# Performance work log

Hardware: AMD Instinct MI355X
Metric: run time of the kernel (lower is better)

## Reference

```python
import jax, jax.numpy as jnp
import numpy as np

B, C, H, W = 32, 4, 512, 512
T = 64  # Angular_representive_Threshold
GROUPS = 2


def setup_inputs() -> dict:
    key = jax.random.key(0)
    k1, k2 = jax.random.split(key)
    x_real = jax.random.normal(k1, (B, C, H, W), dtype=jnp.float32)
    x_imag = jax.random.normal(k2, (B, C, H, W), dtype=jnp.float32)
    return {"x_real": x_real, "x_imag": x_imag}


def reference(x_real, x_imag):
    # Complex angular-delay input, split into 2 groups of 2 channels (torch.chunk dim=1)
    x = (x_real + 1j * x_imag).astype(jnp.complex64)            # [B,4,H,W]
    xg = x.reshape(B, GROUPS, 2, H, W)                          # [B,g,ch,H,W]
    ch0, ch1 = xg[:, :, 0], xg[:, :, 1]                         # [B,g,H,W]
    # sqrt(|real|^2) == |real|; energy difference summed over delay axis H (dim=2)
    diff = (jnp.abs(jnp.abs(ch0.real) - jnp.abs(ch1.imag)) +
            jnp.abs(jnp.abs(ch1.real) - jnp.abs(ch0.imag))).sum(axis=2)  # [B,g,W]
    # torch.sort ascending, keep first T indices (smallest energy difference)
    idx = jnp.argsort(diff, axis=-1)[..., :T]                   # [B,g,T]
    # vectorized column scatter replacing the per-batch/per-threshold python loops
    mask = jnp.zeros((B, GROUPS, W), jnp.float32).at[
        jnp.arange(B)[:, None, None],
        jnp.arange(GROUPS)[None, :, None],
        idx].set(1.0)                                           # [B,g,W]
    xm = xg * mask[:, :, None, None, :]                         # zero non-selected angular bins
    # ifft over delay (dim=-2) then fft over angle (dim=-1), +0.5 on real part
    out = jnp.fft.fft(jnp.fft.ifft(xm, axis=-2), axis=-1) + 0.5
    out = out.reshape(B, C, H, W).astype(jnp.complex64)         # concat of both groups on dim=1
    # return as stacked real/imag float32 (complex64 payload)
    return jnp.stack([out.real, out.imag], axis=-1)             # [B,4,H,W,2]
```

## Files before the change

### kernel.cpp

```cpp
#include <hip/hip_runtime.h>
#include <math.h>

#define NB 32
#define NC 4
#define NH 512
#define NW 512
#define NT 64
#define NG 2
#define BK 32

typedef __attribute__((ext_vector_type(8))) short short8;
typedef __attribute__((ext_vector_type(4))) short short4v;
typedef __attribute__((ext_vector_type(4))) float float4v;

__device__ inline unsigned short f2bf(float f) {
  union { float f; unsigned u; } v; v.f = f;
  unsigned r = v.u + 0x7FFF + ((v.u >> 16) & 1);
  return (unsigned short)(r >> 16);
}

__device__ __forceinline__ void gld16(const unsigned short* g, unsigned short* l) {
  __builtin_amdgcn_global_load_lds(
      (__attribute__((address_space(1))) const unsigned int*)g,
      (__attribute__((address_space(3))) unsigned int*)l, 16, 0, 0);
}

__global__ __launch_bounds__(256) void k_diff(const float* __restrict__ xr,
                                              const float* __restrict__ xi,
                                              float* __restrict__ diffp) {
  int bg = blockIdx.x, hc = blockIdx.y;
  int b = bg >> 1, g = bg & 1;
  size_t c0 = ((size_t)(b * NC + 2 * g)) * NH * NW;
  size_t c1 = c0 + (size_t)NH * NW;
  int t = threadIdx.x;
  int q = t & 127, rg = t >> 7;
  int h0 = hc * 64;
  float4v acc = {0.f, 0.f, 0.f, 0.f};
  for (int r = rg; r < 64; r += 2) {
    size_t o = (size_t)(h0 + r) * NW + q * 4;
    float4v r0 = *(const float4v*)(xr + c0 + o);
    float4v i0 = *(const float4v*)(xi + c0 + o);
    float4v r1 = *(const float4v*)(xr + c1 + o);
    float4v i1 = *(const float4v*)(xi + c1 + o);
#pragma unroll
    for (int k = 0; k < 4; ++k)
      acc[k] += fabsf(fabsf(r0[k]) - fabsf(i1[k])) + fabsf(fabsf(r1[k]) - fabsf(i0[k]));
  }
  __shared__ float4v red[256];
  red[t] = acc;
  __syncthreads();
  if (t < 128) {
    float4v v = red[t];
    float4v u = red[t + 128];
#pragma unroll
    for (int k = 0; k < 4; ++k) v[k] += u[k];
    *(float4v*)(diffp + ((size_t)hc * 64 + bg) * NW + q * 4) = v;
  }
}

__global__ void k_select(const float* __restrict__ diffp, int* __restrict__ sel) {
  __shared__ float v[NW];
  int w = threadIdx.x;
  int bg = blockIdx.x;
  float mine = 0.f;
#pragma unroll
  for (int hc = 0; hc < 8; ++hc) mine += diffp[((size_t)hc * 64 + bg) * NW + w];
  v[w] = mine;
  __syncthreads();
  int rank = 0;
  for (int u = 0; u < NW; ++u) {
    float o = v[u];
    rank += (o < mine) || (o == mine && u < w);
  }
  if (rank < NT) sel[bg * NT + rank] = w;
}

__global__ __launch_bounds__(256) void k_build_T(unsigned short* __restrict__ Tb) {
  __shared__ float2 lt[512];
  int t = threadIdx.x;
  {
    float s, c;
    sincosf(6.2831853071795864769f * (float)t * (1.0f / 512.0f), &s, &c);
    lt[t] = make_float2(c, s);
    sincosf(6.2831853071795864769f * (float)(t + 256) * (1.0f / 512.0f), &s, &c);
    lt[t + 256] = make_float2(c, s);
  }
  __syncthreads();
#pragma unroll
  for (int i = 0; i < 4; ++i) {
    int idx = blockIdx.x * 1024 + i * 256 + t;
    int m = idx >> 10, k = idx & 1023;
    int hm = m & 511, rm = m >> 9;
    int hk = k & 511, rk = k >> 9;
    float2 cs = lt[(hm * hk) & 511];
    float val = (rm == rk) ? cs.x : (rk ? -cs.y : cs.y);
    Tb[idx] = f2bf(val * (1.0f / 512.0f));
  }
}

__global__ __launch_bounds__(256) void k_gather(const float* __restrict__ xr,
                                                const float* __restrict__ xi,
                                                const int* __restrict__ sel,
                                                unsigned short* __restrict__ Xg) {
  __shared__ short jmap[512];
  __shared__ __align__(16) unsigned short tile[2][64][136];
  int img = blockIdx.x, hc = blockIdx.y;
  int t = threadIdx.x;
  int b = img >> 2, g = (img >> 1) & 1;
  jmap[t] = -1;
  jmap[t + 256] = -1;
  __syncthreads();
  if (t < NT) {
    int w = sel[(b * NG + g) * NT + t];
    jmap[w] = (short)t;
  }
  __syncthreads();
  size_t base = (size_t)img * NH * NW + (size_t)hc * 128 * NW;
  for (int i = 0; i < 64; ++i) {
    int lin = i * 256 + t;
    int r = lin >> 7, q = lin & 127;
    size_t o = base + (size_t)r * NW + q * 4;
    float4v vr = *(const float4v*)(xr + o);
    float4v vi = *(const float4v*)(xi + o);
    short4v jm = *(const short4v*)&jmap[q * 4];
#pragma unroll
    for (int k = 0; k < 4; ++k) {
      int j = jm[k];
      if (j >= 0) {
        tile[0][j][r] = f2bf(vr[k]);
        tile[1][j][r] = f2bf(vi[k]);
      }
    }
  }
  __syncthreads();
  int j = t >> 2, s4 = t & 3;
  size_t orow = ((size_t)img * 64 + j) * 1024 + (size_t)hc * 128;
#pragma unroll
  for (int v = 0; v < 4; ++v) {
    int hl = v * 32 + s4 * 8;
    *(short8*)(Xg + orow + hl)       = *(const short8*)&tile[0][j][hl];
    *(short8*)(Xg + orow + 512 + hl) = *(const short8*)&tile[1][j][hl];
  }
}

__global__ __launch_bounds__(256) void k_build_E(const int* __restrict__ sel,
                                                 unsigned short* __restrict__ Eb) {
  __shared__ int wsel[NT];
  __shared__ float2 lt[512];
  int bg = blockIdx.x;
  int t = threadIdx.x;
  {
    float s, c;
    sincosf(6.2831853071795864769f * (float)t * (1.0f / 512.0f), &s, &c);
    lt[t] = make_float2(c, s);
    sincosf(6.2831853071795864769f * (float)(t + 256) * (1.0f / 512.0f), &s, &c);
    lt[t + 256] = make_float2(c, s);
  }
  if (t < NT) wsel[t] = sel[bg * NT + t];
  __syncthreads();
  int base = blockIdx.y * 8192;
#pragma unroll
  for (int i = 0; i < 32; ++i) {
    int idx = base + i * 256 + t;
    int n = idx >> 7, kidx = idx & 127;
    int j = kidx & 63, half = kidx >> 6;
    int part = n >> 9, kk = n & 511;
    int w = wsel[j];
    float2 cs = lt[(kk * w) & 511];
    float val = part == 0 ? (half ? cs.y : cs.x) : (half ? cs.x : -cs.y);
    Eb[(size_t)bg * 131072 + idx] = f2bf(val);
  }
}

__global__ __launch_bounds__(256) void k_gemm3(const unsigned short* __restrict__ Tb,
                                               const unsigned short* __restrict__ Xg,
                                               unsigned short* __restrict__ Yg) {
  __shared__ __align__(16) unsigned short Al[128 * BK];
  __shared__ __align__(16) unsigned short Bl[128 * BK];
  int n0 = blockIdx.x * 128;
  int m0 = blockIdx.y * 128;
  int tid = threadIdx.x;
  int lane = tid & 63, wid = tid >> 6;
  int wm = wid >> 1, wn = wid & 1;
  int quad = lane >> 4, l15 = lane & 15;
  int srow = lane >> 2, sqd = lane & 3;

  float4v acc[4][4];
#pragma unroll
  for (int i = 0; i < 4; ++i)
#pragma unroll
    for (int j = 0; j < 4; ++j) acc[i][j] = (float4v){0.f, 0.f, 0.f, 0.f};

  for (int k0 = 0; k0 < 1024; k0 += BK) {
    __syncthreads();
#pragma unroll
    for (int p = 0; p < 2; ++p) {
      int chunk = wid * 2 + p;
      int row = chunk * 16 + srow;
      int sq = sqd ^ ((row >> 1) & 3);
      gld16(&Tb[(size_t)(m0 + row) * 1024 + k0 + sq * 8], &Al[chunk * 512]);
      gld16(&Xg[(size_t)(n0 + row) * 1024 + k0 + sq * 8], &Bl[chunk * 512]);
    }
    __syncthreads();

    short8 af[4], bfv[4];
#pragma unroll
    for (int tt = 0; tt < 4; ++tt) {
      int ra = wm * 64 + tt * 16 + l15;
      int rb = wn * 64 + tt * 16 + l15;
      af[tt]  = *(const short8*)&Al[ra * BK + ((quad ^ ((ra >> 1) & 3)) << 3)];
      bfv[tt] = *(const short8*)&Bl[rb * BK + ((quad ^ ((rb >> 1) & 3)) << 3)];
    }
#pragma unroll
    for (int tm = 0; tm < 4; ++tm)
#pragma unroll
      for (int tn = 0; tn < 4; ++tn)
        acc[tm][tn] = __builtin_amdgcn_mfma_f32_16x16x32_bf16(af[tm], bfv[tn], acc[tm][tn], 0, 0, 0);
  }

#pragma unroll
  for (int tm = 0; tm < 4; ++tm)
#pragma unroll
    for (int tn = 0; tn < 4; ++tn)
#pragma unroll
      for (int r = 0; r < 4; ++r) {
        int m = m0 + wm * 64 + tm * 16 + quad * 4 + r;
        int n = n0 + wn * 64 + tn * 16 + l15;
        int img = n >> 6, j = n & 63;
        int h = m & 511, ri = m >> 9;
        Yg[((size_t)img * 512 + h) * 128 + ri * 64 + j] = f2bf(acc[tm][tn][r]);
      }
}

__global__ __launch_bounds__(256) void k_gemm4(const unsigned short* __restrict__ Yg,
                                               const unsigned short* __restrict__ Eball,
                                               float2* __restrict__ out) {
  __shared__ __align__(16) unsigned short Al[128 * BK];
  __shared__ __align__(16) unsigned short Bl[128 * BK];
  int n0 = blockIdx.x * 64;
  int m0 = blockIdx.y * 128;
  int bg = blockIdx.z;
  int b = bg >> 1, g = bg & 1;
  int img0 = b * 4 + 2 * g;
  const unsigned short* Ab = Yg + (size_t)img0 * 512 * 128;
  const unsigned short* Eb = Eball + (size_t)bg * 131072;

  int tid = threadIdx.x;
  int lane = tid & 63, wid = tid >> 6;
  int wm = wid >> 1, wn = wid & 1;
  int quad = lane >> 4, l15 = lane & 15;
  int srow = lane >> 2, sqd = lane & 3;

  float4v acc[4][4];
#pragma unroll
  for (int i = 0; i < 4; ++i)
#pragma unroll
    for (int j = 0; j < 4; ++j) acc[i][j] = (float4v){0.f, 0.f, 0.f, 0.f};

  for (int k0 = 0; k0 < 128; k0 += BK) {
    __syncthreads();
#pragma unroll
    for (int p = 0; p < 2; ++p) {
      int chunk = wid * 2 + p;
      int row = chunk * 16 + srow;
      int sq = sqd ^ ((row >> 1) & 3);
      gld16(&Ab[(size_t)(m0 + row) * 128 + k0 + sq * 8], &Al[chunk * 512]);
      int l = row & 63, wnB = row >> 6;
      int part = l >> 5;
      int grow = part * 512 + n0 + wnB * 32 + (l & 31);
      gld16(&Eb[(size_t)grow * 128 + k0 + sq * 8], &Bl[chunk * 512]);
    }
    __syncthreads();

    short8 af[4], bfv[4];
#pragma unroll
    for (int tt = 0; tt < 4; ++tt) {
      int ra = wm * 64 + tt * 16 + l15;
      int rb = wn * 64 + tt * 16 + l15;
      af[tt]  = *(const short8*)&Al[ra * BK + ((quad ^ ((ra >> 1) & 3)) << 3)];
      bfv[tt] = *(const short8*)&Bl[rb * BK + ((quad ^ ((rb >> 1) & 3)) << 3)];
    }
#pragma unroll
    for (int tm = 0; tm < 4; ++tm)
#pragma unroll
      for (int tn = 0; tn < 4; ++tn)
        acc[tm][tn] = __builtin_amdgcn_mfma_f32_16x16x32_bf16(af[tm], bfv[tn], acc[tm][tn], 0, 0, 0);
  }

#pragma unroll
  for (int tm = 0; tm < 4; ++tm)
#pragma unroll
    for (int t2 = 0; t2 < 2; ++t2)
#pragma unroll
      for (int r = 0; r < 4; ++r) {
        int m = m0 + wm * 64 + tm * 16 + quad * 4 + r;
        int ch = m >> 9, h = m & 511;
        int img = img0 + ch;
        int kk = n0 + wn * 32 + t2 * 16 + l15;
        float2 v = make_float2(acc[tm][t2][r] + 0.5f, acc[tm][t2 + 2][r]);
        out[((size_t)(img * 512 + h)) * 512 + kk] = v;
      }
}

extern "C" void kernel_launch(void* const* d_in, const int* in_sizes, int n_in,
                              void* d_out, int out_size, void* d_ws, size_t ws_size,
                              hipStream_t stream) {
  const float* xr = (const float*)d_in[0];
  const float* xi = (const float*)d_in[1];
  float2* out = (float2*)d_out;

  char* ws = (char*)d_ws;
  float*          diffp = (float*)ws;
  int*            sel   = (int*)(ws + 1048576);
  unsigned short* Tb    = (unsigned short*)(ws + 2097152);
  unsigned short* Xg    = (unsigned short*)(ws + 4194304);
  unsigned short* Yg    = (unsigned short*)(ws + 20971520);
  unsigned short* Eb    = (unsigned short*)(ws + 37748736);

  k_diff   <<<dim3(NB * NG, 8), 256, 0, stream>>>(xr, xi, diffp);
  k_select <<<NB * NG,          NW, 0, stream>>>(diffp, sel);
  k_build_T<<<1024,             256, 0, stream>>>(Tb);
  k_gather <<<dim3(NB * NC, 4), 256, 0, stream>>>(xr, xi, sel, Xg);
  k_build_E<<<dim3(NB * NG, 16),256, 0, stream>>>(sel, Eb);
  k_gemm3  <<<dim3(64, 8),      256, 0, stream>>>(Tb, Xg, Yg);
  k_gemm4  <<<dim3(8, 8, 64),   256, 0, stream>>>(Yg, Eb, out);
}
```

Baseline: 589.3 us.

## Double-buffer gemm3 LDS tiles, swizzle block order, load full K in gemm4

k_gemm3 now uses two LDS buffers so global-to-LDS loads for the next K step overlap the MFMA work on the current one, with one barrier per iteration instead of two. Both GEMM kernels remap the linear block index so that neighbouring blocks share operand tiles, aiming for better L2 reuse. k_gemm4 loads its whole K=128 slice into LDS at once with a new XOR swizzle and drops the K loop barriers. The cost is more LDS per block (about 32KB in gemm3 and 64KB in gemm4), which may lower occupancy.

New measurement: 580.0 us. No clear change (-1.6%).

```diff
diff --git a/kernel.cpp b/kernel.cpp
--- a/kernel.cpp
+++ b/kernel.cpp
@@ -175,10 +175,12 @@
 __global__ __launch_bounds__(256) void k_gemm3(const unsigned short* __restrict__ Tb,
                                                const unsigned short* __restrict__ Xg,
                                                unsigned short* __restrict__ Yg) {
-  __shared__ __align__(16) unsigned short Al[128 * BK];
-  __shared__ __align__(16) unsigned short Bl[128 * BK];
-  int n0 = blockIdx.x * 128;
-  int m0 = blockIdx.y * 128;
+  __shared__ __align__(16) unsigned short Al[2][128 * BK];
+  __shared__ __align__(16) unsigned short Bl[2][128 * BK];
+  int lin = blockIdx.y * 64 + blockIdx.x;
+  int swz = (lin & 7) * 64 + (lin >> 3);
+  int n0 = (swz & 63) * 128;
+  int m0 = (swz >> 6) * 128;
   int tid = threadIdx.x;
   int lane = tid & 63, wid = tid >> 6;
   int wm = wid >> 1, wn = wid & 1;
@@ -191,31 +193,40 @@
 #pragma unroll
     for (int j = 0; j < 4; ++j) acc[i][j] = (float4v){0.f, 0.f, 0.f, 0.f};
 
-  for (int k0 = 0; k0 < 1024; k0 += BK) {
-    __syncthreads();
-#pragma unroll
-    for (int p = 0; p < 2; ++p) {
-      int chunk = wid * 2 + p;
-      int row = chunk * 16 + srow;
-      int sq = sqd ^ ((row >> 1) & 3);
-      gld16(&Tb[(size_t)(m0 + row) * 1024 + k0 + sq * 8], &Al[chunk * 512]);
-      gld16(&Xg[(size_t)(n0 + row) * 1024 + k0 + sq * 8], &Bl[chunk * 512]);
-    }
-    __syncthreads();
+#define STAGE3(buf, kk0)                                                        \
+  {                                                                             \
+    _Pragma("unroll")                                                           \
+    for (int p = 0; p < 2; ++p) {                                               \
+      int chunk = wid * 2 + p;                                                  \
+      int row = chunk * 16 + srow;                                              \
+      int sq = sqd ^ ((row >> 1) & 3);                                          \
+      gld16(&Tb[(size_t)(m0 + row) * 1024 + (kk0) + sq * 8], &Al[buf][chunk * 512]); \
+      gld16(&Xg[(size_t)(n0 + row) * 1024 + (kk0) + sq * 8], &Bl[buf][chunk * 512]); \
+    }                                                                           \
+  }
+
+  STAGE3(0, 0);
+  __syncthreads();
+  int cur = 0;
+  for (int t = 0; t < 32; ++t) {
+    if (t < 31) STAGE3(cur ^ 1, (t + 1) * 32);
 
     short8 af[4], bfv[4];
 #pragma unroll
     for (int tt = 0; tt < 4; ++tt) {
       int ra = wm * 64 + tt * 16 + l15;
       int rb = wn * 64 + tt * 16 + l15;
-      af[tt]  = *(const short8*)&Al[ra * BK + ((quad ^ ((ra >> 1) & 3)) << 3)];
-      bfv[tt] = *(const short8*)&Bl[rb * BK + ((quad ^ ((rb >> 1) & 3)) << 3)];
+      af[tt]  = *(const short8*)&Al[cur][ra * BK + ((quad ^ ((ra >> 1) & 3)) << 3)];
+      bfv[tt] = *(const short8*)&Bl[cur][rb * BK + ((quad ^ ((rb >> 1) & 3)) << 3)];
     }
 #pragma unroll
     for (int tm = 0; tm < 4; ++tm)
 #pragma unroll
       for (int tn = 0; tn < 4; ++tn)
         acc[tm][tn] = __builtin_amdgcn_mfma_f32_16x16x32_bf16(af[tm], bfv[tn], acc[tm][tn], 0, 0, 0);
+
+    __syncthreads();
+    cur ^= 1;
   }
 
 #pragma unroll
@@ -235,11 +246,13 @@
 __global__ __launch_bounds__(256) void k_gemm4(const unsigned short* __restrict__ Yg,
                                                const unsigned short* __restrict__ Eball,
                                                float2* __restrict__ out) {
-  __shared__ __align__(16) unsigned short Al[128 * BK];
-  __shared__ __align__(16) unsigned short Bl[128 * BK];
-  int n0 = blockIdx.x * 64;
-  int m0 = blockIdx.y * 128;
-  int bg = blockIdx.z;
+  __shared__ __align__(16) unsigned short Al[128 * 128];
+  __shared__ __align__(16) unsigned short Bl[128 * 128];
+  int lin = blockIdx.x + blockIdx.y * 8 + blockIdx.z * 64;
+  int swz = (lin & 7) * 512 + (lin >> 3);
+  int n0 = (swz & 7) * 64;
+  int m0 = ((swz >> 3) & 7) * 128;
+  int bg = swz >> 6;
   int b = bg >> 1, g = bg & 1;
   int img0 = b * 4 + 2 * g;
   const unsigned short* Ab = Yg + (size_t)img0 * 512 * 128;
@@ -249,7 +262,20 @@
   int lane = tid & 63, wid = tid >> 6;
   int wm = wid >> 1, wn = wid & 1;
   int quad = lane >> 4, l15 = lane & 15;
-  int srow = lane >> 2, sqd = lane & 3;
+  int lrow4 = lane >> 4, cch = lane & 15;
+
+#pragma unroll
+  for (int c8 = 0; c8 < 8; ++c8) {
+    int call = wid * 8 + c8;
+    int row = call * 4 + lrow4;
+    int sch = cch ^ (row & 7);
+    gld16(&Ab[(size_t)(m0 + row) * 128 + sch * 8], &Al[call * 512]);
+    int l = row & 63, wnB = row >> 6;
+    int part = l >> 5;
+    int grow = part * 512 + n0 + wnB * 32 + (l & 31);
+    gld16(&Eb[(size_t)grow * 128 + sch * 8], &Bl[call * 512]);
+  }
+  __syncthreads();
 
   float4v acc[4][4];
 #pragma unroll
@@ -257,28 +283,15 @@
 #pragma unroll
     for (int j = 0; j < 4; ++j) acc[i][j] = (float4v){0.f, 0.f, 0.f, 0.f};
 
-  for (int k0 = 0; k0 < 128; k0 += BK) {
-    __syncthreads();
-#pragma unroll
-    for (int p = 0; p < 2; ++p) {
-      int chunk = wid * 2 + p;
-      int row = chunk * 16 + srow;
-      int sq = sqd ^ ((row >> 1) & 3);
-      gld16(&Ab[(size_t)(m0 + row) * 128 + k0 + sq * 8], &Al[chunk * 512]);
-      int l = row & 63, wnB = row >> 6;
-      int part = l >> 5;
-      int grow = part * 512 + n0 + wnB * 32 + (l & 31);
-      gld16(&Eb[(size_t)grow * 128 + k0 + sq * 8], &Bl[chunk * 512]);
-    }
-    __syncthreads();
-
+#pragma unroll
+  for (int ks = 0; ks < 4; ++ks) {
     short8 af[4], bfv[4];
 #pragma unroll
     for (int tt = 0; tt < 4; ++tt) {
       int ra = wm * 64 + tt * 16 + l15;
       int rb = wn * 64 + tt * 16 + l15;
-      af[tt]  = *(const short8*)&Al[ra * BK + ((quad ^ ((ra >> 1) & 3)) << 3)];
-      bfv[tt] = *(const short8*)&Bl[rb * BK + ((quad ^ ((rb >> 1) & 3)) << 3)];
+      af[tt]  = *(const short8*)&Al[ra * 128 + (((ks * 4 + quad) ^ (ra & 7)) << 3)];
+      bfv[tt] = *(const short8*)&Bl[rb * 128 + (((ks * 4 + quad) ^ (rb & 7)) << 3)];
     }
 #pragma unroll
     for (int tm = 0; tm < 4; ++tm)
```
